# Kernel optimization log

Measured on AMD Instinct MI355X. Metric: run time of the kernel, lower is better.

The kernel has to match this reference:

```python
import jax, jax.numpy as jnp
import numpy as np

N = 50000      # nodes
E = 1600000    # random edges (self-loops appended)
D = 128        # feature_size
C = 300        # n_content_dims


def setup_inputs() -> dict:
    key = jax.random.key(0)
    ks = jax.random.split(key, 8)
    src = jax.random.randint(ks[0], (E,), 0, N, dtype=jnp.int32)
    dst = jax.random.randint(ks[1], (E,), 0, N, dtype=jnp.int32)
    loop = jnp.arange(N, dtype=jnp.int32)
    edge_src = jnp.concatenate([src, loop])  # [E+N]
    edge_dst = jnp.concatenate([dst, loop])
    content = jax.random.normal(ks[2], (N, C), dtype=jnp.float32)
    node_emb = jax.random.normal(ks[3], (N + 1, D), dtype=jnp.float32) * (1.0 / D)
    proj_W = jax.random.normal(ks[4], (D, C), dtype=jnp.float32) * float(1.0 / np.sqrt(C))
    proj_b = jnp.zeros((D,), jnp.float32)
    W1 = jax.random.normal(ks[5], (D, 2 * D), jnp.float32) * float(1.0 / np.sqrt(2 * D))
    b1 = jnp.zeros((D,), jnp.float32)
    W2 = jax.random.normal(ks[6], (D, 2 * D), jnp.float32) * float(1.0 / np.sqrt(2 * D))
    b2 = jnp.zeros((D,), jnp.float32)
    return dict(node_emb=node_emb, content=content, proj_W=proj_W, proj_b=proj_b,
                W1=W1, b1=b1, W2=W2, b2=b2, edge_src=edge_src, edge_dst=edge_dst)


def _sage_conv(h, edge_src, edge_dst, W, b, use_act):
    # DGL copy_src('h')/sum -> h_agg ; copy_src('one')/sum -> w (in-degree)
    h_agg = jax.ops.segment_sum(h[edge_src], edge_dst, num_segments=N)  # [N, D]
    w = jax.ops.segment_sum(jnp.ones((edge_src.shape[0],), h.dtype), edge_dst, num_segments=N)
    h_agg = (h_agg - h) / jnp.maximum(w - 1.0, 1.0)[:, None]  # exclude self, mean over neighbors
    h_new = jnp.concatenate([h, h_agg], axis=1) @ W.T + b     # [N, D]
    if use_act:
        h_new = jax.nn.leaky_relu(h_new, 0.1)
    norm = jnp.linalg.norm(h_new, axis=1, keepdims=True)
    return h_new / jnp.maximum(norm, 1e-6)


def reference(node_emb, content, proj_W, proj_b, W1, b1, W2, b2, edge_src, edge_dst):
    ids = jnp.arange(N, dtype=jnp.int32)
    # node embedding (ids offset by +1) + LeakyReLU content projection (mix_embeddings)
    h = node_emb[ids + 1] + jax.nn.leaky_relu(content @ proj_W.T + proj_b, 0.1)
    h = _sage_conv(h, edge_src, edge_dst, W1, b1, True)   # intermediate layer: leaky_relu
    h = _sage_conv(h, edge_src, edge_dst, W2, b2, False)  # last layer: linear activation
    return h
```

## Files before the change

### kernel.cpp

```cpp
#include <hip/hip_runtime.h>

#define Nn 50000
#define Dd 128
#define Cc 300

#define BIN_SHIFT 7
#define BIN_W (1 << BIN_SHIFT)
#define NBINS ((Nn + BIN_W - 1) >> BIN_SHIFT)
#define CAP 5120
#define SCHUNK 8192

typedef __bf16 bf16_t;
typedef bf16_t bf16x8 __attribute__((ext_vector_type(8)));
typedef float f32x4 __attribute__((ext_vector_type(4)));
typedef unsigned u32x4 __attribute__((ext_vector_type(4)));
typedef unsigned u32x2 __attribute__((ext_vector_type(2)));

__device__ __forceinline__ float lrelu(float x) { return x > 0.f ? x : 0.1f * x; }

__device__ __forceinline__ unsigned f2bf(float f) {
    unsigned u = __builtin_bit_cast(unsigned, f);
    return (u + 0x7fffu + ((u >> 16) & 1u)) >> 16;
}
__device__ __forceinline__ unsigned pack2(float a, float b) {
    return f2bf(a) | (f2bf(b) << 16);
}
__device__ __forceinline__ float bflo(unsigned v) {
    return __builtin_bit_cast(float, v << 16);
}
__device__ __forceinline__ float bfhi(unsigned v) {
    return __builtin_bit_cast(float, v & 0xffff0000u);
}


__global__ __launch_bounds__(512) void k_binscatter(const int* __restrict__ esrc,
                                                    const int* __restrict__ edst,
                                                    int* __restrict__ binCursor,
                                                    unsigned* __restrict__ pairs, int ET) {
    __shared__ unsigned sorted[SCHUNK];
    __shared__ int hist[NBINS];
    __shared__ int lbase[NBINS];
    __shared__ int gbase[NBINS];
    __shared__ int wsums[8];
    int tid = threadIdx.x;
    int c0 = blockIdx.x * SCHUNK;
    int n = min(SCHUNK, ET - c0);
    for (int i = tid; i < NBINS; i += 512) hist[i] = 0;
    __syncthreads();
    for (int i = tid; i < n; i += 512)
        atomicAdd(&hist[((unsigned)edst[c0 + i]) >> BIN_SHIFT], 1);
    __syncthreads();
    {
        int lane = tid & 63, wid = tid >> 6;
        int v = (tid < NBINS) ? hist[tid] : 0;
        int incl = v;
        #pragma unroll
        for (int off = 1; off < 64; off <<= 1) {
            int t = __shfl_up(incl, off, 64);
            if (lane >= off) incl += t;
        }
        if (lane == 63) wsums[wid] = incl;
        __syncthreads();
        if (tid == 0) {
            int run = 0;
            #pragma unroll
            for (int w = 0; w < 8; ++w) { int t = wsums[w]; wsums[w] = run; run += t; }
        }
        __syncthreads();
        if (tid < NBINS) {
            int excl = wsums[wid] + incl - v;
            lbase[tid] = excl;
            gbase[tid] = v ? atomicAdd(&binCursor[tid], v) : 0;
            hist[tid] = 0;
        }
    }
    __syncthreads();
    for (int i = tid; i < n; i += 512) {
        unsigned s = (unsigned)esrc[c0 + i];
        unsigned d = (unsigned)edst[c0 + i];
        unsigned b = d >> BIN_SHIFT;
        unsigned pk = s | ((d & (BIN_W - 1)) << 16) | (b << 23);
        int pos = lbase[b] + atomicAdd(&hist[b], 1);
        sorted[pos] = pk;
    }
    __syncthreads();
    for (int i = tid; i < n; i += 512) {
        unsigned pk = sorted[i];
        unsigned b = pk >> 23;
        int idx = gbase[b] + (i - lbase[b]);
        if (idx < CAP)
            pairs[(size_t)b * CAP + idx] = pk & 0x7fffffu;
    }
}

__global__ __launch_bounds__(256) void k_binsort(const unsigned* __restrict__ pairs,
                                                 const int* __restrict__ binCursor,
                                                 int* __restrict__ offs,
                                                 int* __restrict__ deg,
                                                 int* __restrict__ bucket) {
    __shared__ int cnt[BIN_W];
    __shared__ int cur[BIN_W];
    __shared__ int srcbuf[CAP];
    __shared__ int w0sum;
    int bin = blockIdx.x;
    int e0 = bin * CAP;
    int n = min(binCursor[bin], CAP);
    int tid = threadIdx.x;
    if (tid < BIN_W) cnt[tid] = 0;
    __syncthreads();
    const unsigned* p2 = pairs + e0;
    for (int i = tid; i < n; i += 256)
        atomicAdd(&cnt[p2[i] >> 16], 1);
    __syncthreads();
    int v = 0, incl = 0;
    if (tid < BIN_W) {
        v = cnt[tid];
        incl = v;
        #pragma unroll
        for (int off = 1; off < 64; off <<= 1) {
            int t = __shfl_up(incl, off, 64);
            if ((tid & 63) >= off) incl += t;
        }
    }
    if (tid == 63) w0sum = incl;
    __syncthreads();
    if (tid < BIN_W) {
        int excl = incl - v + (tid >= 64 ? w0sum : 0);
        cur[tid] = excl;
        int node = (bin << BIN_SHIFT) + tid;
        if (node < Nn) {
            __builtin_nontemporal_store(e0 + excl, &offs[node]);
            __builtin_nontemporal_store(v, &deg[node]);
        }
    }
    __syncthreads();
    for (int i = tid; i < n; i += 256) {
        unsigned pr = p2[i];
        int p = atomicAdd(&cur[pr >> 16], 1);
        if (p < CAP) srcbuf[p] = (int)(pr & 0xffffu);
    }
    __syncthreads();
    for (int i = tid; i < n; i += 256)
        __builtin_nontemporal_store(srcbuf[i], &bucket[e0 + i]);
}


__global__ __launch_bounds__(256) void k_agg(const unsigned short* __restrict__ h,
                                             const int* __restrict__ offs,
                                             const int* __restrict__ deg,
                                             const int* __restrict__ bucket,
                                             unsigned short* __restrict__ agg) {
    int node = blockIdx.x * 4 + (threadIdx.x >> 6);
    if (node >= Nn) return;
    int lane = threadIdx.x & 63;
    const unsigned* h1 = (const unsigned*)h;
    int s = offs[node], d = deg[node];
    float ax = 0.f, ay = 0.f;
    for (int base = 0; base < d; base += 64) {
        int nrem = min(64, d - base);
        int myid = 0;
        if (base + lane < d) myid = bucket[s + base + lane];
        int j = 0;
        for (; j + 8 <= nrem; j += 8) {
            int i0 = __shfl(myid, j + 0), i1 = __shfl(myid, j + 1);
            int i2 = __shfl(myid, j + 2), i3 = __shfl(myid, j + 3);
            int i4 = __shfl(myid, j + 4), i5 = __shfl(myid, j + 5);
            int i6 = __shfl(myid, j + 6), i7 = __shfl(myid, j + 7);
            unsigned v0 = h1[(size_t)i0 * 64 + lane];
            unsigned v1 = h1[(size_t)i1 * 64 + lane];
            unsigned v2 = h1[(size_t)i2 * 64 + lane];
            unsigned v3 = h1[(size_t)i3 * 64 + lane];
            unsigned v4 = h1[(size_t)i4 * 64 + lane];
            unsigned v5 = h1[(size_t)i5 * 64 + lane];
            unsigned v6 = h1[(size_t)i6 * 64 + lane];
            unsigned v7 = h1[(size_t)i7 * 64 + lane];
            ax += ((bflo(v0) + bflo(v1)) + (bflo(v2) + bflo(v3))) +
                  ((bflo(v4) + bflo(v5)) + (bflo(v6) + bflo(v7)));
            ay += ((bfhi(v0) + bfhi(v1)) + (bfhi(v2) + bfhi(v3))) +
                  ((bfhi(v4) + bfhi(v5)) + (bfhi(v6) + bfhi(v7)));
        }
        for (; j < nrem; ++j) {
            int id = __shfl(myid, j);
            unsigned v = h1[(size_t)id * 64 + lane];
            ax += bflo(v);
            ay += bfhi(v);
        }
    }
    unsigned self = h1[(size_t)node * 64 + lane];
    float inv = 1.f / fmaxf((float)d - 1.f, 1.f);
    ax = (ax - bflo(self)) * inv;
    ay = (ay - bfhi(self)) * inv;
    __builtin_nontemporal_store(pack2(ax, ay), &((unsigned*)agg)[(size_t)node * 64 + lane]);
}


__device__ __forceinline__ bf16x8 ldfrag(const unsigned short* sm, int row, int ks, int lg) {
    unsigned g = (unsigned)((ks * 4 + lg) ^ (row & 7));
    return __builtin_bit_cast(bf16x8, *(const u32x4*)(sm + row * 64 + g * 8));
}
__device__ __forceinline__ void st8(unsigned short* sm, int row, int c4, unsigned lo, unsigned hi) {
    unsigned off = (unsigned)row * 64 + ((((unsigned)c4 >> 1) ^ (row & 7)) << 3) + ((c4 & 1) << 2);
    *(u32x2*)(sm + off) = (u32x2){lo, hi};
}


__global__ __launch_bounds__(256) void k_h0(const float* __restrict__ content,
                                            const float* __restrict__ projW,
                                            const float* __restrict__ projB,
                                            const float* __restrict__ emb,
                                            unsigned short* __restrict__ h) {
    __shared__ unsigned short sA[64 * 64];
    __shared__ unsigned short sB[128 * 64];
    int bm = blockIdx.x * 64;
    int tid = threadIdx.x;
    int wid = tid >> 6, l = tid & 63, lr = l & 15, lg = l >> 4;
    int wm = (wid & 1) * 32, wn = (wid >> 1) * 64;
    f32x4 acc[2][4];
    #pragma unroll
    for (int mf = 0; mf < 2; ++mf)
        #pragma unroll
        for (int nf = 0; nf < 4; ++nf) acc[mf][nf] = (f32x4){0.f, 0.f, 0.f, 0.f};

    for (int k0 = 0; k0 < 320; k0 += 64) {
        for (int idx = tid; idx < 64 * 16; idx += 256) {
            int r = idx >> 4, c4 = idx & 15;
            int gi = bm + r, k = k0 + c4 * 4;
            float4 v = make_float4(0.f, 0.f, 0.f, 0.f);
            if (gi < Nn && k < Cc) v = *(const float4*)(content + (size_t)gi * Cc + k);
            st8(sA, r, c4, pack2(v.x, v.y), pack2(v.z, v.w));
        }
        for (int idx = tid; idx < 128 * 16; idx += 256) {
            int r = idx >> 4, c4 = idx & 15;
            int k = k0 + c4 * 4;
            float4 v = make_float4(0.f, 0.f, 0.f, 0.f);
            if (k < Cc) v = *(const float4*)(projW + (size_t)r * Cc + k);
            st8(sB, r, c4, pack2(v.x, v.y), pack2(v.z, v.w));
        }
        __syncthreads();
        #pragma unroll
        for (int ks = 0; ks < 2; ++ks) {
            bf16x8 a[2], b[4];
            #pragma unroll
            for (int mf = 0; mf < 2; ++mf) a[mf] = ldfrag(sA, wm + mf * 16 + lr, ks, lg);
            #pragma unroll
            for (int nf = 0; nf < 4; ++nf) b[nf] = ldfrag(sB, wn + nf * 16 + lr, ks, lg);
            #pragma unroll
            for (int mf = 0; mf < 2; ++mf)
                #pragma unroll
                for (int nf = 0; nf < 4; ++nf)
                    acc[mf][nf] = __builtin_amdgcn_mfma_f32_16x16x32_bf16(a[mf], b[nf], acc[mf][nf], 0, 0, 0);
        }
        __syncthreads();
    }

    float pb[4];
    #pragma unroll
    for (int nf = 0; nf < 4; ++nf) pb[nf] = projB[wn + nf * 16 + lr];
    #pragma unroll
    for (int mf = 0; mf < 2; ++mf)
        #pragma unroll
        for (int v = 0; v < 4; ++v) {
            int row = bm + wm + mf * 16 + lg * 4 + v;
            if (row >= Nn) continue;
            #pragma unroll
            for (int nf = 0; nf < 4; ++nf) {
                int col = wn + nf * 16 + lr;
                float x = lrelu(acc[mf][nf][v] + pb[nf]) + emb[(size_t)(row + 1) * Dd + col];
                h[(size_t)row * Dd + col] = (unsigned short)f2bf(x);
            }
        }
}


template <int MODE>
__global__ __launch_bounds__(256) void k_layer(const unsigned short* __restrict__ hsrc,
                                               const unsigned short* __restrict__ asrc,
                                               const float* __restrict__ W,
                                               const float* __restrict__ bias,
                                               void* __restrict__ outp) {
    __shared__ unsigned short sA[64 * 64];
    __shared__ unsigned short sB[128 * 64];
    __shared__ float rowsum[64];
    int bm = blockIdx.x * 64;
    int tid = threadIdx.x;
    int wid = tid >> 6, l = tid & 63, lr = l & 15, lg = l >> 4;
    int wm = (wid & 1) * 32, wn = (wid >> 1) * 64;
    if (tid < 64) rowsum[tid] = 0.f;
    f32x4 acc[2][4];
    #pragma unroll
    for (int mf = 0; mf < 2; ++mf)
        #pragma unroll
        for (int nf = 0; nf < 4; ++nf) acc[mf][nf] = (f32x4){0.f, 0.f, 0.f, 0.f};

    for (int kc = 0; kc < 4; ++kc) {
        const unsigned short* Asrc = (kc < 2) ? hsrc : asrc;
        int koff = (kc & 1) * 64;
        for (int idx = tid; idx < 64 * 8; idx += 256) {
            int r = idx >> 3, g = idx & 7;
            int gi = bm + r;
            u32x4 v = (u32x4){0u, 0u, 0u, 0u};
            if (gi < Nn) v = *(const u32x4*)(Asrc + (size_t)gi * Dd + koff + g * 8);
            unsigned gg = (unsigned)g ^ (r & 7);
            *(u32x4*)(sA + r * 64 + gg * 8) = v;
        }
        for (int idx = tid; idx < 128 * 16; idx += 256) {
            int r = idx >> 4, c4 = idx & 15;
            int k = kc * 64 + c4 * 4;
            float4 v = *(const float4*)(W + (size_t)r * 256 + k);
            st8(sB, r, c4, pack2(v.x, v.y), pack2(v.z, v.w));
        }
        __syncthreads();
        #pragma unroll
        for (int ks = 0; ks < 2; ++ks) {
            bf16x8 a[2], b[4];
            #pragma unroll
            for (int mf = 0; mf < 2; ++mf) a[mf] = ldfrag(sA, wm + mf * 16 + lr, ks, lg);
            #pragma unroll
            for (int nf = 0; nf < 4; ++nf) b[nf] = ldfrag(sB, wn + nf * 16 + lr, ks, lg);
            #pragma unroll
            for (int mf = 0; mf < 2; ++mf)
                #pragma unroll
                for (int nf = 0; nf < 4; ++nf)
                    acc[mf][nf] = __builtin_amdgcn_mfma_f32_16x16x32_bf16(a[mf], b[nf], acc[mf][nf], 0, 0, 0);
        }
        __syncthreads();
    }

    float pb[4];
    #pragma unroll
    for (int nf = 0; nf < 4; ++nf) pb[nf] = bias[wn + nf * 16 + lr];
    float ps[2][4];
    #pragma unroll
    for (int mf = 0; mf < 2; ++mf)
        #pragma unroll
        for (int v = 0; v < 4; ++v) {
            float s = 0.f;
            #pragma unroll
            for (int nf = 0; nf < 4; ++nf) {
                float x = acc[mf][nf][v] + pb[nf];
                if (MODE == 0) x = lrelu(x);
                acc[mf][nf][v] = x;
                s += x * x;
            }
            ps[mf][v] = s;
        }
    #pragma unroll
    for (int off = 1; off < 16; off <<= 1)
        #pragma unroll
        for (int mf = 0; mf < 2; ++mf)
            #pragma unroll
            for (int v = 0; v < 4; ++v) ps[mf][v] += __shfl_xor(ps[mf][v], off, 16);
    if (lr == 0) {
        #pragma unroll
        for (int mf = 0; mf < 2; ++mf)
            #pragma unroll
            for (int v = 0; v < 4; ++v)
                atomicAdd(&rowsum[wm + mf * 16 + lg * 4 + v], ps[mf][v]);
    }
    __syncthreads();
    #pragma unroll
    for (int mf = 0; mf < 2; ++mf)
        #pragma unroll
        for (int v = 0; v < 4; ++v) {
            int row = bm + wm + mf * 16 + lg * 4 + v;
            if (row >= Nn) continue;
            float inv = 1.f / fmaxf(sqrtf(rowsum[wm + mf * 16 + lg * 4 + v]), 1e-6f);
            #pragma unroll
            for (int nf = 0; nf < 4; ++nf) {
                int col = wn + nf * 16 + lr;
                float x = acc[mf][nf][v] * inv;
                if (MODE == 0)
                    ((unsigned short*)outp)[(size_t)row * Dd + col] = (unsigned short)f2bf(x);
                else
                    ((float*)outp)[(size_t)row * Dd + col] = x;
            }
        }
}


extern "C" void kernel_launch(void* const* d_in, const int* in_sizes, int n_in,
                              void* d_out, int out_size, void* d_ws, size_t ws_size,
                              hipStream_t stream) {
    const float* node_emb = (const float*)d_in[0];
    const float* content  = (const float*)d_in[1];
    const float* projW    = (const float*)d_in[2];
    const float* projB    = (const float*)d_in[3];
    const float* W1 = (const float*)d_in[4];
    const float* b1 = (const float*)d_in[5];
    const float* W2 = (const float*)d_in[6];
    const float* b2 = (const float*)d_in[7];
    const int* esrc = (const int*)d_in[8];
    const int* edst = (const int*)d_in[9];
    const int ET = in_sizes[8];
    float* out = (float*)d_out;

    unsigned short* h0  = (unsigned short*)d_ws;
    unsigned short* h1  = h0 + (size_t)Nn * Dd;
    unsigned short* agg = h1 + (size_t)Nn * Dd;
    int* offs      = (int*)(agg + (size_t)Nn * Dd);
    int* deg       = offs + Nn;
    int* binCursor = deg + Nn;
    int* bucket    = binCursor + NBINS;
    unsigned* pairs = (unsigned*)(bucket + (size_t)NBINS * CAP);

    hipMemsetAsync(binCursor, 0, NBINS * sizeof(int), stream);
    k_binscatter<<<(ET + SCHUNK - 1) / SCHUNK, 512, 0, stream>>>(esrc, edst, binCursor, pairs, ET);
    k_binsort<<<NBINS, 256, 0, stream>>>(pairs, binCursor, offs, deg, bucket);

    k_h0<<<(Nn + 63) / 64, 256, 0, stream>>>(content, projW, projB, node_emb, h0);

    k_agg<<<(Nn + 3) / 4, 256, 0, stream>>>(h0, offs, deg, bucket, agg);
    k_layer<0><<<(Nn + 63) / 64, 256, 0, stream>>>(h0, agg, W1, b1, (void*)h1);

    k_agg<<<(Nn + 3) / 4, 256, 0, stream>>>(h1, offs, deg, bucket, agg);
    k_layer<1><<<(Nn + 63) / 64, 256, 0, stream>>>(h1, agg, W2, b2, (void*)out);
}
```

Baseline: 353.6 us.

## Load content directly into MFMA registers, stage full projW once, batch agg gathers

The content-projection kernel now converts the whole projection weight matrix to bf16 in shared memory once per block. It then reads content rows straight from global memory into MFMA A fragments, which removes the per-K-step shared-memory staging and the barriers around it. The aggregation kernel issues up to 16 gathered loads before accumulating, to raise memory-level parallelism, and loads the self row first. It also switches the output to an ordinary store instead of a nontemporal one. The larger shared buffer (80KB) may reduce occupancy, and the direct A loads are less coalesced.

```diff
diff --git a/kernel.cpp b/kernel.cpp
--- a/kernel.cpp
+++ b/kernel.cpp
@@ -30,6 +30,10 @@
 }
 __device__ __forceinline__ float bfhi(unsigned v) {
     return __builtin_bit_cast(float, v & 0xffff0000u);
+}
+__device__ __forceinline__ bf16x8 cvt8(float4 a, float4 b) {
+    u32x4 r = {pack2(a.x, a.y), pack2(a.z, a.w), pack2(b.x, b.y), pack2(b.z, b.w)};
+    return __builtin_bit_cast(bf16x8, r);
 }
 
 
@@ -154,43 +158,34 @@
     if (node >= Nn) return;
     int lane = threadIdx.x & 63;
     const unsigned* h1 = (const unsigned*)h;
+    unsigned self = h1[(size_t)node * 64 + lane];
     int s = offs[node], d = deg[node];
     float ax = 0.f, ay = 0.f;
     for (int base = 0; base < d; base += 64) {
         int nrem = min(64, d - base);
         int myid = 0;
         if (base + lane < d) myid = bucket[s + base + lane];
-        int j = 0;
-        for (; j + 8 <= nrem; j += 8) {
-            int i0 = __shfl(myid, j + 0), i1 = __shfl(myid, j + 1);
-            int i2 = __shfl(myid, j + 2), i3 = __shfl(myid, j + 3);
-            int i4 = __shfl(myid, j + 4), i5 = __shfl(myid, j + 5);
-            int i6 = __shfl(myid, j + 6), i7 = __shfl(myid, j + 7);
-            unsigned v0 = h1[(size_t)i0 * 64 + lane];
-            unsigned v1 = h1[(size_t)i1 * 64 + lane];
-            unsigned v2 = h1[(size_t)i2 * 64 + lane];
-            unsigned v3 = h1[(size_t)i3 * 64 + lane];
-            unsigned v4 = h1[(size_t)i4 * 64 + lane];
-            unsigned v5 = h1[(size_t)i5 * 64 + lane];
-            unsigned v6 = h1[(size_t)i6 * 64 + lane];
-            unsigned v7 = h1[(size_t)i7 * 64 + lane];
-            ax += ((bflo(v0) + bflo(v1)) + (bflo(v2) + bflo(v3))) +
-                  ((bflo(v4) + bflo(v5)) + (bflo(v6) + bflo(v7)));
-            ay += ((bfhi(v0) + bfhi(v1)) + (bfhi(v2) + bfhi(v3))) +
-                  ((bfhi(v4) + bfhi(v5)) + (bfhi(v6) + bfhi(v7)));
-        }
-        for (; j < nrem; ++j) {
-            int id = __shfl(myid, j);
-            unsigned v = h1[(size_t)id * 64 + lane];
-            ax += bflo(v);
-            ay += bfhi(v);
-        }
-    }
-    unsigned self = h1[(size_t)node * 64 + lane];
+        for (int j = 0; j < nrem; j += 16) {
+            int cnt = min(16, nrem - j);
+            unsigned v[16];
+            #pragma unroll
+            for (int t = 0; t < 16; ++t)
+                if (t < cnt) {
+                    int id = __shfl(myid, j + t);
+                    v[t] = h1[(size_t)id * 64 + lane];
+                }
+            #pragma unroll
+            for (int t = 0; t < 16; ++t)
+                if (t < cnt) {
+                    ax += bflo(v[t]);
+                    ay += bfhi(v[t]);
+                }
+        }
+    }
     float inv = 1.f / fmaxf((float)d - 1.f, 1.f);
     ax = (ax - bflo(self)) * inv;
     ay = (ay - bfhi(self)) * inv;
-    __builtin_nontemporal_store(pack2(ax, ay), &((unsigned*)agg)[(size_t)node * 64 + lane]);
+    ((unsigned*)agg)[(size_t)node * 64 + lane] = pack2(ax, ay);
 }
 
 
@@ -209,48 +204,81 @@
                                             const float* __restrict__ projB,
                                             const float* __restrict__ emb,
                                             unsigned short* __restrict__ h) {
-    __shared__ unsigned short sA[64 * 64];
-    __shared__ unsigned short sB[128 * 64];
+    __shared__ unsigned short sB[128 * 320];
     int bm = blockIdx.x * 64;
     int tid = threadIdx.x;
     int wid = tid >> 6, l = tid & 63, lr = l & 15, lg = l >> 4;
     int wm = (wid & 1) * 32, wn = (wid >> 1) * 64;
+
+    for (int idx = tid; idx < 128 * 40; idx += 256) {
+        int r = idx / 40, g = idx % 40;
+        int k = g * 8;
+        float4 v0 = make_float4(0.f, 0.f, 0.f, 0.f), v1 = v0;
+        if (k + 8 <= Cc) {
+            v0 = *(const float4*)(projW + (size_t)r * Cc + k);
+            v1 = *(const float4*)(projW + (size_t)r * Cc + k + 4);
+        } else if (k + 4 <= Cc) {
+            v0 = *(const float4*)(projW + (size_t)r * Cc + k);
+        }
+        unsigned g2 = (unsigned)g ^ (r & 7);
+        *(u32x4*)(sB + r * 320 + g2 * 8) =
+            (u32x4){pack2(v0.x, v0.y), pack2(v0.z, v0.w), pack2(v1.x, v1.y), pack2(v1.z, v1.w)};
+    }
+    __syncthreads();
+
     f32x4 acc[2][4];
     #pragma unroll
     for (int mf = 0; mf < 2; ++mf)
         #pragma unroll
         for (int nf = 0; nf < 4; ++nf) acc[mf][nf] = (f32x4){0.f, 0.f, 0.f, 0.f};
 
-    for (int k0 = 0; k0 < 320; k0 += 64) {
-        for (int idx = tid; idx < 64 * 16; idx += 256) {
-            int r = idx >> 4, c4 = idx & 15;
-            int gi = bm + r, k = k0 + c4 * 4;
-            float4 v = make_float4(0.f, 0.f, 0.f, 0.f);
-            if (gi < Nn && k < Cc) v = *(const float4*)(content + (size_t)gi * Cc + k);
-            st8(sA, r, c4, pack2(v.x, v.y), pack2(v.z, v.w));
-        }
-        for (int idx = tid; idx < 128 * 16; idx += 256) {
-            int r = idx >> 4, c4 = idx & 15;
-            int k = k0 + c4 * 4;
-            float4 v = make_float4(0.f, 0.f, 0.f, 0.f);
-            if (k < Cc) v = *(const float4*)(projW + (size_t)r * Cc + k);
-            st8(sB, r, c4, pack2(v.x, v.y), pack2(v.z, v.w));
-        }
-        __syncthreads();
-        #pragma unroll
-        for (int ks = 0; ks < 2; ++ks) {
-            bf16x8 a[2], b[4];
-            #pragma unroll
-            for (int mf = 0; mf < 2; ++mf) a[mf] = ldfrag(sA, wm + mf * 16 + lr, ks, lg);
-            #pragma unroll
-            for (int nf = 0; nf < 4; ++nf) b[nf] = ldfrag(sB, wn + nf * 16 + lr, ks, lg);
-            #pragma unroll
-            for (int mf = 0; mf < 2; ++mf)
-                #pragma unroll
-                for (int nf = 0; nf < 4; ++nf)
-                    acc[mf][nf] = __builtin_amdgcn_mfma_f32_16x16x32_bf16(a[mf], b[nf], acc[mf][nf], 0, 0, 0);
-        }
-        __syncthreads();
+    int row0 = bm + wm + lr;
+    int row1 = row0 + 16;
+    bool ok0 = row0 < Nn, ok1 = row1 < Nn;
+    const float* a0p = content + (size_t)row0 * Cc + lg * 8;
+    const float* a1p = content + (size_t)row1 * Cc + lg * 8;
+    const float4 z4 = make_float4(0.f, 0.f, 0.f, 0.f);
+    const bf16x8 az = __builtin_bit_cast(bf16x8, (u32x4){0u, 0u, 0u, 0u});
+
+    #pragma unroll 3
+    for (int ks = 0; ks < 9; ++ks) {
+        bf16x8 a0 = az, a1 = az;
+        if (ok0) a0 = cvt8(*(const float4*)(a0p + ks * 32), *(const float4*)(a0p + ks * 32 + 4));
+        if (ok1) a1 = cvt8(*(const float4*)(a1p + ks * 32), *(const float4*)(a1p + ks * 32 + 4));
+        bf16x8 b[4];
+        #pragma unroll
+        for (int nf = 0; nf < 4; ++nf) {
+            int rw = wn + nf * 16 + lr;
+            unsigned g2 = (unsigned)(ks * 4 + lg) ^ (rw & 7);
+            b[nf] = __builtin_bit_cast(bf16x8, *(const u32x4*)(sB + rw * 320 + g2 * 8));
+        }
+        #pragma unroll
+        for (int nf = 0; nf < 4; ++nf) {
+            acc[0][nf] = __builtin_amdgcn_mfma_f32_16x16x32_bf16(a0, b[nf], acc[0][nf], 0, 0, 0);
+            acc[1][nf] = __builtin_amdgcn_mfma_f32_16x16x32_bf16(a1, b[nf], acc[1][nf], 0, 0, 0);
+        }
+    }
+    {
+        bf16x8 a0 = az, a1 = az;
+        if (lg == 0) {
+            if (ok0) a0 = cvt8(*(const float4*)(a0p + 288), *(const float4*)(a0p + 292));
+            if (ok1) a1 = cvt8(*(const float4*)(a1p + 288), *(const float4*)(a1p + 292));
+        } else if (lg == 1) {
+            if (ok0) a0 = cvt8(*(const float4*)(a0p + 288), z4);
+            if (ok1) a1 = cvt8(*(const float4*)(a1p + 288), z4);
+        }
+        bf16x8 b[4];
+        #pragma unroll
+        for (int nf = 0; nf < 4; ++nf) {
+            int rw = wn + nf * 16 + lr;
+            unsigned g2 = (unsigned)(9 * 4 + lg) ^ (rw & 7);
+            b[nf] = __builtin_bit_cast(bf16x8, *(const u32x4*)(sB + rw * 320 + g2 * 8));
+        }
+        #pragma unroll
+        for (int nf = 0; nf < 4; ++nf) {
+            acc[0][nf] = __builtin_amdgcn_mfma_f32_16x16x32_bf16(a0, b[nf], acc[0][nf], 0, 0, 0);
+            acc[1][nf] = __builtin_amdgcn_mfma_f32_16x16x32_bf16(a1, b[nf], acc[1][nf], 0, 0, 0);
+        }
     }
 
     float pb[4];
```

New measurement: 475.2 us. +34.4%, slower.
